# Kernel tuning notes

Hardware: AMD Instinct MI355X
Metric: run time of the kernel (lower is better)

Reference implementation:

```python
import jax, jax.numpy as jnp
import numpy as np

ATT_DIM = 128
C = 256
B, H, W = 4, 64, 64


def setup_inputs() -> dict:
    key = jax.random.key(0)
    ks = jax.random.split(key, 6)
    s = 1.0 / np.sqrt(C)
    return {
        "x": jax.random.normal(ks[0], (B, C, H, W), dtype=jnp.float32),
        "Wg": jax.random.normal(ks[1], (ATT_DIM, C), dtype=jnp.float32) * s,
        "Wf": jax.random.normal(ks[2], (ATT_DIM, C), dtype=jnp.float32) * s,
        "Wh": jax.random.normal(ks[3], (ATT_DIM, C), dtype=jnp.float32) * s,
        "Wv": jax.random.normal(ks[4], (C, ATT_DIM), dtype=jnp.float32) * (1.0 / np.sqrt(ATT_DIM)),
        "lambda_att": jax.random.normal(ks[5], (), dtype=jnp.float32),
    }


def reference(x, Wg, Wf, Wh, Wv, lambda_att):
    # x: [B, C, H, W]; 1x1 channels_first convs == channel matmuls
    b, c, h, w = x.shape
    hw = h * w
    d = Wg.shape[0]
    # project and flatten spatial dims -> tokens: [B, HW, d]
    g = jnp.einsum('dc,bchw->bhwd', Wg, x).reshape(b, hw, d)  # query
    f = jnp.einsum('dc,bchw->bhwd', Wf, x).reshape(b, hw, d)  # value
    hh = jnp.einsum('dc,bchw->bhwd', Wh, x).reshape(b, hw, d)  # key
    # keras layers.Attention([g, f, h]): scores = query @ key^T (unscaled),
    # out = softmax(scores) @ value
    scores = jnp.einsum('bqd,bkd->bqk', g, hh)  # [B, HW, HW]
    attw = jax.nn.softmax(scores, axis=-1)
    v = jnp.einsum('bqk,bkd->bqd', attw, f)  # [B, HW, d]
    # back to [B, d, H, W], project to C channels
    v = v.transpose(0, 2, 1).reshape(b, d, h, w)
    v = jnp.einsum('cd,bdhw->bchw', Wv, v)
    return x + lambda_att * v
```

## Files before the change

### kernel.cpp

```cpp
#include <hip/hip_runtime.h>

typedef _Float16 h16;
typedef __attribute__((ext_vector_type(8))) _Float16 half8;
typedef __attribute__((ext_vector_type(4))) _Float16 half4;
typedef __attribute__((ext_vector_type(4))) float f32x4;
typedef unsigned int u32;
typedef unsigned short u16;
typedef unsigned long long u64;

#define LOG2E 1.44269504088896340736f

__device__ __forceinline__ void gl_lds16(const void* g, void* l){
  __builtin_amdgcn_global_load_lds((const __attribute__((address_space(1))) u32*)g,
                                   (__attribute__((address_space(3))) u32*)l, 16, 0, 0);
}
__device__ __forceinline__ f32x4 mfma16(half8 a, half8 b, f32x4 c){
  return __builtin_amdgcn_mfma_f32_16x16x32_f16(a, b, c, 0, 0, 0);
}
__device__ __forceinline__ f32x4 fzero(){
  f32x4 z = {0.f, 0.f, 0.f, 0.f};
  return z;
}

__global__ void k_cvtw(const float* __restrict__ Wg, const float* __restrict__ Wf,
                       const float* __restrict__ Wh, const float* __restrict__ Wv,
                       h16* __restrict__ o){
  int i = blockIdx.x * 256 + threadIdx.x;
  o[i]          = (h16)Wg[i];
  o[32768 + i]  = (h16)Wf[i];
  o[65536 + i]  = (h16)Wh[i];
  o[98304 + i]  = (h16)Wv[i];
}

__global__ __launch_bounds__(256, 2)
void k_proj(const float* __restrict__ x, const h16* __restrict__ Wgb,
            const h16* __restrict__ Whb, const h16* __restrict__ Wfb,
            h16* __restrict__ Q, h16* __restrict__ K, h16* __restrict__ Vt){
  __shared__ __align__(16) char Xl[64 * 512];
  int bid = blockIdx.x;
  int b = bid >> 6, p0 = (bid & 63) * 64;
  int tid = threadIdx.x;
  int w = tid >> 6, lane = tid & 63, g4 = lane >> 4, ln = lane & 15;

  #pragma unroll
  for (int pass = 0; pass < 4; ++pass){
    int idx = pass * 256 + tid;
    int c4 = idx >> 4, p4 = idx & 15;
    const float* xp = x + ((size_t)b * 256 + c4 * 4) * 4096 + p0 + p4 * 4;
    float4 v0 = *(const float4*)(xp);
    float4 v1 = *(const float4*)(xp + 4096);
    float4 v2 = *(const float4*)(xp + 8192);
    float4 v3 = *(const float4*)(xp + 12288);
    #pragma unroll
    for (int i = 0; i < 4; ++i){
      int row = p4 * 4 + i;
      half4 v = { (h16)((&v0.x)[i]), (h16)((&v1.x)[i]),
                  (h16)((&v2.x)[i]), (h16)((&v3.x)[i]) };
      *(half4*)&Xl[row * 512 + ((c4 * 8) ^ ((row & 7) << 4))] = v;
    }
  }
  __syncthreads();

  half8 xf[4][8];
  #pragma unroll
  for (int pt = 0; pt < 4; ++pt){
    int p = pt * 16 + ln;
    #pragma unroll
    for (int ks = 0; ks < 8; ++ks)
      xf[pt][ks] = *(const half8*)&Xl[p * 512 + (((ks * 4 + g4) ^ (p & 7)) << 4)];
  }

  const h16* Ws0[3] = {Wgb, Whb, Wfb};
  #pragma unroll
  for (int mat = 0; mat < 3; ++mat){
    const h16* Wm = Ws0[mat];
    #pragma unroll
    for (int dtl = 0; dtl < 2; ++dtl){
      int drow = w * 32 + dtl * 16 + ln;
      half8 wf[8];
      #pragma unroll
      for (int ks = 0; ks < 8; ++ks)
        wf[ks] = *(const half8*)&Wm[(size_t)drow * 256 + ks * 32 + g4 * 8];
      #pragma unroll
      for (int pt = 0; pt < 4; ++pt){
        f32x4 acc = fzero();
        #pragma unroll
        for (int ks = 0; ks < 8; ++ks)
          acc = mfma16(wf[ks], xf[pt][ks], acc);
        int p = p0 + pt * 16 + ln;
        int dbase = w * 32 + dtl * 16 + g4 * 4;
        if (mat < 2){
          h16* Dst = (mat == 0) ? Q : K;
          half4 v = { (h16)acc[0], (h16)acc[1], (h16)acc[2], (h16)acc[3] };
          *(half4*)&Dst[((size_t)b * 4096 + p) * 128 + dbase] = v;
        } else {
          #pragma unroll
          for (int r = 0; r < 4; ++r)
            Vt[((size_t)b * 128 + dbase + r) * 4096 + p] = (h16)acc[r];
        }
      }
    }
  }
}

__global__ __launch_bounds__(128, 2)
void k_attn(const h16* __restrict__ Q, const h16* __restrict__ K,
            const h16* __restrict__ Vt, h16* __restrict__ Opart,
            float* __restrict__ Mb, float* __restrict__ Lb){
  __shared__ __align__(16) char Kl[16384];
  __shared__ __align__(16) char Vl[16384];
  __shared__ __align__(16) char Pl[2][4096];

  int bid = blockIdx.x;
  int b = bid >> 8, qb = (bid >> 2) & 63, sp = bid & 3;
  int tid = threadIdx.x;
  int w = tid >> 6, lane = tid & 63, g4 = lane >> 4, ln = lane & 15;
  int q0 = qb * 64 + w * 32;

  half8 qf[2][4];
  #pragma unroll
  for (int qt = 0; qt < 2; ++qt)
    #pragma unroll
    for (int ks = 0; ks < 4; ++ks)
      qf[qt][ks] = *(const half8*)&Q[((size_t)b * 4096 + q0 + qt * 16 + ln) * 128 + ks * 32 + g4 * 8];

  f32x4 acc[2][8];
  #pragma unroll
  for (int qt = 0; qt < 2; ++qt)
    #pragma unroll
    for (int dt = 0; dt < 8; ++dt)
      acc[qt][dt] = fzero();
  float mrow[2] = {-1e30f, -1e30f};
  float lrow[2] = {0.f, 0.f};

  for (int t = 0; t < 16; ++t){
    int kv0 = sp * 1024 + t * 64;
    __syncthreads();
    #pragma unroll
    for (int i = 0; i < 8; ++i){
      int off = i * 2048 + w * 1024 + lane * 16;
      int row = off >> 8, c16 = (off >> 4) & 15;
      gl_lds16(&K[((size_t)b * 4096 + kv0 + row) * 128 + ((c16 ^ (row & 7)) << 3)],
               &Kl[i * 2048 + w * 1024]);
    }
    #pragma unroll
    for (int i = 0; i < 8; ++i){
      int off = i * 2048 + w * 1024 + lane * 16;
      int row = off >> 7, c16 = (off >> 4) & 7;
      gl_lds16(&Vt[((size_t)b * 128 + row) * 4096 + kv0 + ((c16 ^ (row & 7)) << 3)],
               &Vl[i * 2048 + w * 1024]);
    }
    __syncthreads();

    f32x4 s[4][2];
    #pragma unroll
    for (int kt = 0; kt < 4; ++kt)
      #pragma unroll
      for (int qt = 0; qt < 2; ++qt) s[kt][qt] = fzero();
    #pragma unroll
    for (int kt = 0; kt < 4; ++kt){
      int key = kt * 16 + ln;
      #pragma unroll
      for (int ks = 0; ks < 4; ++ks){
        half8 kf = *(const half8*)&Kl[key * 256 + (((ks * 4 + g4) ^ (key & 7)) << 4)];
        #pragma unroll
        for (int qt = 0; qt < 2; ++qt)
          s[kt][qt] = mfma16(kf, qf[qt][ks], s[kt][qt]);
      }
    }

    #pragma unroll
    for (int qt = 0; qt < 2; ++qt){
      float mx = -1e30f;
      #pragma unroll
      for (int kt = 0; kt < 4; ++kt)
        #pragma unroll
        for (int r = 0; r < 4; ++r) mx = fmaxf(mx, s[kt][qt][r]);
      mx = fmaxf(mx, __shfl_xor(mx, 16));
      mx = fmaxf(mx, __shfl_xor(mx, 32));
      float mnew = fmaxf(mrow[qt], mx);
      float scale = exp2f((mrow[qt] - mnew) * LOG2E);
      mrow[qt] = mnew;
      float ps = 0.f;
      int q = qt * 16 + ln;
      #pragma unroll
      for (int kt = 0; kt < 4; ++kt){
        float e0 = exp2f((s[kt][qt][0] - mnew) * LOG2E);
        float e1 = exp2f((s[kt][qt][1] - mnew) * LOG2E);
        float e2 = exp2f((s[kt][qt][2] - mnew) * LOG2E);
        float e3 = exp2f((s[kt][qt][3] - mnew) * LOG2E);
        ps += (e0 + e1) + (e2 + e3);
        half4 pv = { (h16)e0, (h16)e1, (h16)e2, (h16)e3 };
        *(half4*)&Pl[w][q * 128 + ((kt * 32 + g4 * 8) ^ ((q & 7) << 4))] = pv;
      }
      ps += __shfl_xor(ps, 16);
      ps += __shfl_xor(ps, 32);
      lrow[qt] = lrow[qt] * scale + ps;
      #pragma unroll
      for (int r = 0; r < 4; ++r){
        float sc = __shfl(scale, g4 * 4 + r);
        #pragma unroll
        for (int dt = 0; dt < 8; ++dt) acc[qt][dt][r] *= sc;
      }
    }

    #pragma unroll
    for (int st = 0; st < 2; ++st){
      half8 pa[2];
      #pragma unroll
      for (int qt = 0; qt < 2; ++qt){
        int q = qt * 16 + ln;
        pa[qt] = *(const half8*)&Pl[w][q * 128 + (((st * 4 + g4) ^ (q & 7)) << 4)];
      }
      #pragma unroll
      for (int dt = 0; dt < 8; ++dt){
        int row = dt * 16 + ln;
        half8 vf = *(const half8*)&Vl[row * 128 + (((st * 4 + g4) ^ (row & 7)) << 4)];
        #pragma unroll
        for (int qt = 0; qt < 2; ++qt)
          acc[qt][dt] = mfma16(pa[qt], vf, acc[qt][dt]);
      }
    }
  }

  int pb = (b * 64 + qb) * 4 + sp;
  #pragma unroll
  for (int qt = 0; qt < 2; ++qt)
    #pragma unroll
    for (int dt = 0; dt < 8; ++dt)
      #pragma unroll
      for (int r = 0; r < 4; ++r){
        int qloc = w * 32 + qt * 16 + g4 * 4 + r;
        Opart[(size_t)pb * 8192 + qloc * 128 + dt * 16 + ln] = (h16)acc[qt][dt][r];
      }
  if (lane < 16){
    #pragma unroll
    for (int qt = 0; qt < 2; ++qt){
      int qloc = w * 32 + qt * 16 + lane;
      Mb[pb * 64 + qloc] = mrow[qt];
      Lb[pb * 64 + qloc] = lrow[qt];
    }
  }
}

__global__ __launch_bounds__(256, 4)
void k_comb(const h16* __restrict__ Opart, const float* __restrict__ Mb,
            const float* __restrict__ Lb, h16* __restrict__ O){
  int bid = blockIdx.x;
  int b = bid >> 6, qb = bid & 63;
  int tid = threadIdx.x;
  int q = tid >> 2, dg = tid & 3;
  int base = bid * 4;
  float m0 = Mb[(base + 0) * 64 + q], m1 = Mb[(base + 1) * 64 + q];
  float m2 = Mb[(base + 2) * 64 + q], m3 = Mb[(base + 3) * 64 + q];
  float mmax = fmaxf(fmaxf(m0, m1), fmaxf(m2, m3));
  float w0 = exp2f((m0 - mmax) * LOG2E), w1 = exp2f((m1 - mmax) * LOG2E);
  float w2 = exp2f((m2 - mmax) * LOG2E), w3 = exp2f((m3 - mmax) * LOG2E);
  float denom = w0 * Lb[(base + 0) * 64 + q] + w1 * Lb[(base + 1) * 64 + q]
              + w2 * Lb[(base + 2) * 64 + q] + w3 * Lb[(base + 3) * 64 + q];
  float inv = 1.f / denom;
  #pragma unroll
  for (int d8 = 0; d8 < 4; ++d8){
    int d = dg * 32 + d8 * 8;
    half8 a0 = *(const half8*)&Opart[((size_t)(base + 0) * 64 + q) * 128 + d];
    half8 a1 = *(const half8*)&Opart[((size_t)(base + 1) * 64 + q) * 128 + d];
    half8 a2 = *(const half8*)&Opart[((size_t)(base + 2) * 64 + q) * 128 + d];
    half8 a3 = *(const half8*)&Opart[((size_t)(base + 3) * 64 + q) * 128 + d];
    half8 o;
    #pragma unroll
    for (int j = 0; j < 8; ++j){
      float v = w0 * (float)a0[j] + w1 * (float)a1[j]
              + w2 * (float)a2[j] + w3 * (float)a3[j];
      o[j] = (h16)(v * inv);
    }
    *(half8*)&O[((size_t)b * 4096 + qb * 64 + q) * 128 + d] = o;
  }
}

__global__ __launch_bounds__(256, 2)
void k_oproj(const float* __restrict__ x, const h16* __restrict__ Wvb,
             const h16* __restrict__ O, const float* __restrict__ lamp,
             float* __restrict__ y){
  __shared__ __align__(16) char Ol[16384];
  int bid = blockIdx.x;
  int b = bid >> 6, p0 = (bid & 63) * 64;
  int tid = threadIdx.x;
  int w = tid >> 6, lane = tid & 63, g4 = lane >> 4, ln = lane & 15;
  float lam = lamp[0];

  #pragma unroll
  for (int i = 0; i < 4; ++i){
    int off = i * 4096 + w * 1024 + lane * 16;
    int row = off >> 8, c16 = (off >> 4) & 15;
    gl_lds16(&O[((size_t)b * 4096 + p0 + row) * 128 + ((c16 ^ (row & 7)) << 3)],
             &Ol[i * 4096 + w * 1024]);
  }
  __syncthreads();

  half8 of[4][4];
  #pragma unroll
  for (int pt = 0; pt < 4; ++pt){
    int p = pt * 16 + ln;
    #pragma unroll
    for (int ks = 0; ks < 4; ++ks)
      of[pt][ks] = *(const half8*)&Ol[p * 256 + (((ks * 4 + g4) ^ (p & 7)) << 4)];
  }
  #pragma unroll
  for (int ctl = 0; ctl < 4; ++ctl){
    int crow = w * 64 + ctl * 16 + ln;
    half8 wf[4];
    #pragma unroll
    for (int ks = 0; ks < 4; ++ks)
      wf[ks] = *(const half8*)&Wvb[(size_t)crow * 128 + ks * 32 + g4 * 8];
    #pragma unroll
    for (int pt = 0; pt < 4; ++pt){
      f32x4 a = fzero();
      #pragma unroll
      for (int ks = 0; ks < 4; ++ks) a = mfma16(wf[ks], of[pt][ks], a);
      int p = p0 + pt * 16 + ln;
      int c = w * 64 + ctl * 16 + g4 * 4;
      #pragma unroll
      for (int r = 0; r < 4; ++r){
        size_t idx = ((size_t)b * 256 + c + r) * 4096 + p;
        y[idx] = x[idx] + lam * a[r];
      }
    }
  }
}

extern "C" void kernel_launch(void* const* d_in, const int* in_sizes, int n_in,
                              void* d_out, int out_size, void* d_ws, size_t ws_size,
                              hipStream_t stream) {
  const float* x   = (const float*)d_in[0];
  const float* Wg  = (const float*)d_in[1];
  const float* Wf  = (const float*)d_in[2];
  const float* Wh  = (const float*)d_in[3];
  const float* Wv  = (const float*)d_in[4];
  const float* lam = (const float*)d_in[5];

  h16* Wall  = (h16*)d_ws;
  h16* Qb    = Wall + 131072;
  h16* Kb    = Qb + 2097152;
  h16* Vtb   = Kb + 2097152;
  h16* Ob    = Vtb + 2097152;
  h16* Opart = Ob + 2097152;
  float* Mb  = (float*)(Opart + 8388608);
  float* Lb  = Mb + 65536;

  k_cvtw<<<128, 256, 0, stream>>>(Wg, Wf, Wh, Wv, Wall);
  k_proj<<<256, 256, 0, stream>>>(x, Wall , Wall + 65536 , Wall + 32768 ,
                                  Qb, Kb, Vtb);
  k_attn<<<1024, 128, 0, stream>>>(Qb, Kb, Vtb, Opart, Mb, Lb);
  k_comb<<<256, 256, 0, stream>>>(Opart, Mb, Lb, Ob);
  k_oproj<<<256, 256, 0, stream>>>(x, Wall + 98304 , Ob, lam, (float*)d_out);
}
```

Baseline: 163.2 us.

## Double-buffer K tiles, read V from global, lazy rescale, fuse combine into oproj

The attention kernel now runs 4 waves of 16 query rows each. K tiles are double-buffered in LDS so the next tile's load overlaps compute, and V is read straight from global memory instead of being staged. Softmax rescaling is skipped unless the row max grows by more than 8, and partial outputs are normalized before being written. The split-combine kernel is folded into the output projection, which removes one launch and the O round trip. Reading V from global adds uncached global traffic, and the lazy-rescale threshold lets fp16 probabilities reach e^8, which is within fp16 range.

```diff
diff --git a/kernel.cpp b/kernel.cpp
--- a/kernel.cpp
+++ b/kernel.cpp
@@ -5,7 +5,6 @@
 typedef __attribute__((ext_vector_type(4))) _Float16 half4;
 typedef __attribute__((ext_vector_type(4))) float f32x4;
 typedef unsigned int u32;
-typedef unsigned short u16;
 typedef unsigned long long u64;
 
 #define LOG2E 1.44269504088896340736f
@@ -103,208 +102,169 @@
   }
 }
 
-__global__ __launch_bounds__(128, 2)
+__global__ __launch_bounds__(256, 4)
 void k_attn(const h16* __restrict__ Q, const h16* __restrict__ K,
             const h16* __restrict__ Vt, h16* __restrict__ Opart,
             float* __restrict__ Mb, float* __restrict__ Lb){
-  __shared__ __align__(16) char Kl[16384];
-  __shared__ __align__(16) char Vl[16384];
-  __shared__ __align__(16) char Pl[2][4096];
+  __shared__ __align__(16) char Kl[2][16384];
+  __shared__ __align__(16) char Pl[4][2048];
 
   int bid = blockIdx.x;
   int b = bid >> 8, qb = (bid >> 2) & 63, sp = bid & 3;
   int tid = threadIdx.x;
   int w = tid >> 6, lane = tid & 63, g4 = lane >> 4, ln = lane & 15;
-  int q0 = qb * 64 + w * 32;
-
-  half8 qf[2][4];
-  #pragma unroll
-  for (int qt = 0; qt < 2; ++qt)
-    #pragma unroll
-    for (int ks = 0; ks < 4; ++ks)
-      qf[qt][ks] = *(const half8*)&Q[((size_t)b * 4096 + q0 + qt * 16 + ln) * 128 + ks * 32 + g4 * 8];
-
-  f32x4 acc[2][8];
-  #pragma unroll
-  for (int qt = 0; qt < 2; ++qt)
-    #pragma unroll
-    for (int dt = 0; dt < 8; ++dt)
-      acc[qt][dt] = fzero();
-  float mrow[2] = {-1e30f, -1e30f};
-  float lrow[2] = {0.f, 0.f};
-
-  for (int t = 0; t < 16; ++t){
-    int kv0 = sp * 1024 + t * 64;
-    __syncthreads();
-    #pragma unroll
-    for (int i = 0; i < 8; ++i){
-      int off = i * 2048 + w * 1024 + lane * 16;
+  int q0 = qb * 64 + w * 16;
+
+  half8 qf[4];
+  #pragma unroll
+  for (int ks = 0; ks < 4; ++ks)
+    qf[ks] = *(const half8*)&Q[((size_t)b * 4096 + q0 + ln) * 128 + ks * 32 + g4 * 8];
+
+  f32x4 acc[8];
+  #pragma unroll
+  for (int dt = 0; dt < 8; ++dt) acc[dt] = fzero();
+  float mrow = -1e30f, lrow = 0.f;
+
+  int base0 = sp * 1024;
+  const h16* vb = Vt + (size_t)b * 128 * 4096;
+
+  auto stage = [&](int buf, int kv0){
+    #pragma unroll
+    for (int i = 0; i < 4; ++i){
+      int off = i * 4096 + w * 1024 + lane * 16;
       int row = off >> 8, c16 = (off >> 4) & 15;
       gl_lds16(&K[((size_t)b * 4096 + kv0 + row) * 128 + ((c16 ^ (row & 7)) << 3)],
-               &Kl[i * 2048 + w * 1024]);
-    }
-    #pragma unroll
-    for (int i = 0; i < 8; ++i){
-      int off = i * 2048 + w * 1024 + lane * 16;
-      int row = off >> 7, c16 = (off >> 4) & 7;
-      gl_lds16(&Vt[((size_t)b * 128 + row) * 4096 + kv0 + ((c16 ^ (row & 7)) << 3)],
-               &Vl[i * 2048 + w * 1024]);
-    }
-    __syncthreads();
-
-    f32x4 s[4][2];
-    #pragma unroll
-    for (int kt = 0; kt < 4; ++kt)
-      #pragma unroll
-      for (int qt = 0; qt < 2; ++qt) s[kt][qt] = fzero();
+               &Kl[buf][i * 4096 + w * 1024]);
+    }
+  };
+
+  stage(0, base0);
+  __syncthreads();
+
+  int cur = 0;
+  for (int t = 0; t < 16; ++t){
+    int kv0 = base0 + t * 64;
+    if (t < 15) stage(cur ^ 1, kv0 + 64);
+
+    f32x4 s[4];
+    #pragma unroll
+    for (int kt = 0; kt < 4; ++kt) s[kt] = fzero();
     #pragma unroll
     for (int kt = 0; kt < 4; ++kt){
       int key = kt * 16 + ln;
       #pragma unroll
       for (int ks = 0; ks < 4; ++ks){
-        half8 kf = *(const half8*)&Kl[key * 256 + (((ks * 4 + g4) ^ (key & 7)) << 4)];
-        #pragma unroll
-        for (int qt = 0; qt < 2; ++qt)
-          s[kt][qt] = mfma16(kf, qf[qt][ks], s[kt][qt]);
-      }
-    }
-
-    #pragma unroll
-    for (int qt = 0; qt < 2; ++qt){
-      float mx = -1e30f;
-      #pragma unroll
-      for (int kt = 0; kt < 4; ++kt)
-        #pragma unroll
-        for (int r = 0; r < 4; ++r) mx = fmaxf(mx, s[kt][qt][r]);
-      mx = fmaxf(mx, __shfl_xor(mx, 16));
-      mx = fmaxf(mx, __shfl_xor(mx, 32));
-      float mnew = fmaxf(mrow[qt], mx);
-      float scale = exp2f((mrow[qt] - mnew) * LOG2E);
-      mrow[qt] = mnew;
-      float ps = 0.f;
-      int q = qt * 16 + ln;
-      #pragma unroll
-      for (int kt = 0; kt < 4; ++kt){
-        float e0 = exp2f((s[kt][qt][0] - mnew) * LOG2E);
-        float e1 = exp2f((s[kt][qt][1] - mnew) * LOG2E);
-        float e2 = exp2f((s[kt][qt][2] - mnew) * LOG2E);
-        float e3 = exp2f((s[kt][qt][3] - mnew) * LOG2E);
-        ps += (e0 + e1) + (e2 + e3);
-        half4 pv = { (h16)e0, (h16)e1, (h16)e2, (h16)e3 };
-        *(half4*)&Pl[w][q * 128 + ((kt * 32 + g4 * 8) ^ ((q & 7) << 4))] = pv;
-      }
-      ps += __shfl_xor(ps, 16);
-      ps += __shfl_xor(ps, 32);
-      lrow[qt] = lrow[qt] * scale + ps;
+        half8 kf = *(const half8*)&Kl[cur][key * 256 + (((ks * 4 + g4) ^ (key & 7)) << 4)];
+        s[kt] = mfma16(kf, qf[ks], s[kt]);
+      }
+    }
+
+    float mx = -1e30f;
+    #pragma unroll
+    for (int kt = 0; kt < 4; ++kt)
+      #pragma unroll
+      for (int r = 0; r < 4; ++r) mx = fmaxf(mx, s[kt][r]);
+    mx = fmaxf(mx, __shfl_xor(mx, 16));
+    mx = fmaxf(mx, __shfl_xor(mx, 32));
+    if (!__all(mx <= mrow + 8.f)){
+      float mnew = fmaxf(mrow, mx);
+      float scale = exp2f((mrow - mnew) * LOG2E);
+      lrow *= scale;
       #pragma unroll
       for (int r = 0; r < 4; ++r){
         float sc = __shfl(scale, g4 * 4 + r);
         #pragma unroll
-        for (int dt = 0; dt < 8; ++dt) acc[qt][dt][r] *= sc;
-      }
-    }
+        for (int dt = 0; dt < 8; ++dt) acc[dt][r] *= sc;
+      }
+      mrow = mnew;
+    }
+    float ps = 0.f;
+    #pragma unroll
+    for (int kt = 0; kt < 4; ++kt){
+      float e0 = exp2f((s[kt][0] - mrow) * LOG2E);
+      float e1 = exp2f((s[kt][1] - mrow) * LOG2E);
+      float e2 = exp2f((s[kt][2] - mrow) * LOG2E);
+      float e3 = exp2f((s[kt][3] - mrow) * LOG2E);
+      ps += (e0 + e1) + (e2 + e3);
+      half4 pv = { (h16)e0, (h16)e1, (h16)e2, (h16)e3 };
+      *(half4*)&Pl[w][ln * 128 + ((kt * 32 + g4 * 8) ^ ((ln & 7) << 4))] = pv;
+    }
+    ps += __shfl_xor(ps, 16);
+    ps += __shfl_xor(ps, 32);
+    lrow += ps;
 
     #pragma unroll
     for (int st = 0; st < 2; ++st){
-      half8 pa[2];
-      #pragma unroll
-      for (int qt = 0; qt < 2; ++qt){
-        int q = qt * 16 + ln;
-        pa[qt] = *(const half8*)&Pl[w][q * 128 + (((st * 4 + g4) ^ (q & 7)) << 4)];
-      }
+      half8 pa = *(const half8*)&Pl[w][ln * 128 + (((st * 4 + g4) ^ (ln & 7)) << 4)];
       #pragma unroll
       for (int dt = 0; dt < 8; ++dt){
-        int row = dt * 16 + ln;
-        half8 vf = *(const half8*)&Vl[row * 128 + (((st * 4 + g4) ^ (row & 7)) << 4)];
-        #pragma unroll
-        for (int qt = 0; qt < 2; ++qt)
-          acc[qt][dt] = mfma16(pa[qt], vf, acc[qt][dt]);
-      }
-    }
-  }
-
+        half8 vf = *(const half8*)&vb[((size_t)(dt * 16 + ln)) * 4096 + kv0 + st * 32 + g4 * 8];
+        acc[dt] = mfma16(pa, vf, acc[dt]);
+      }
+    }
+
+    __syncthreads();
+    cur ^= 1;
+  }
+
+  float inv = 1.f / lrow;
   int pb = (b * 64 + qb) * 4 + sp;
   #pragma unroll
-  for (int qt = 0; qt < 2; ++qt)
+  for (int r = 0; r < 4; ++r){
+    float invr = __shfl(inv, g4 * 4 + r);
+    int qloc = w * 16 + g4 * 4 + r;
     #pragma unroll
     for (int dt = 0; dt < 8; ++dt)
-      #pragma unroll
-      for (int r = 0; r < 4; ++r){
-        int qloc = w * 32 + qt * 16 + g4 * 4 + r;
-        Opart[(size_t)pb * 8192 + qloc * 128 + dt * 16 + ln] = (h16)acc[qt][dt][r];
-      }
+      Opart[(size_t)pb * 8192 + qloc * 128 + dt * 16 + ln] = (h16)(acc[dt][r] * invr);
+  }
   if (lane < 16){
-    #pragma unroll
-    for (int qt = 0; qt < 2; ++qt){
-      int qloc = w * 32 + qt * 16 + lane;
-      Mb[pb * 64 + qloc] = mrow[qt];
-      Lb[pb * 64 + qloc] = lrow[qt];
-    }
-  }
-}
-
-__global__ __launch_bounds__(256, 4)
-void k_comb(const h16* __restrict__ Opart, const float* __restrict__ Mb,
-            const float* __restrict__ Lb, h16* __restrict__ O){
-  int bid = blockIdx.x;
-  int b = bid >> 6, qb = bid & 63;
-  int tid = threadIdx.x;
-  int q = tid >> 2, dg = tid & 3;
-  int base = bid * 4;
-  float m0 = Mb[(base + 0) * 64 + q], m1 = Mb[(base + 1) * 64 + q];
-  float m2 = Mb[(base + 2) * 64 + q], m3 = Mb[(base + 3) * 64 + q];
-  float mmax = fmaxf(fmaxf(m0, m1), fmaxf(m2, m3));
-  float w0 = exp2f((m0 - mmax) * LOG2E), w1 = exp2f((m1 - mmax) * LOG2E);
-  float w2 = exp2f((m2 - mmax) * LOG2E), w3 = exp2f((m3 - mmax) * LOG2E);
-  float denom = w0 * Lb[(base + 0) * 64 + q] + w1 * Lb[(base + 1) * 64 + q]
-              + w2 * Lb[(base + 2) * 64 + q] + w3 * Lb[(base + 3) * 64 + q];
-  float inv = 1.f / denom;
-  #pragma unroll
-  for (int d8 = 0; d8 < 4; ++d8){
-    int d = dg * 32 + d8 * 8;
-    half8 a0 = *(const half8*)&Opart[((size_t)(base + 0) * 64 + q) * 128 + d];
-    half8 a1 = *(const half8*)&Opart[((size_t)(base + 1) * 64 + q) * 128 + d];
-    half8 a2 = *(const half8*)&Opart[((size_t)(base + 2) * 64 + q) * 128 + d];
-    half8 a3 = *(const half8*)&Opart[((size_t)(base + 3) * 64 + q) * 128 + d];
-    half8 o;
-    #pragma unroll
-    for (int j = 0; j < 8; ++j){
-      float v = w0 * (float)a0[j] + w1 * (float)a1[j]
-              + w2 * (float)a2[j] + w3 * (float)a3[j];
-      o[j] = (h16)(v * inv);
-    }
-    *(half8*)&O[((size_t)b * 4096 + qb * 64 + q) * 128 + d] = o;
+    Mb[pb * 64 + w * 16 + lane] = mrow;
+    Lb[pb * 64 + w * 16 + lane] = lrow;
   }
 }
 
 __global__ __launch_bounds__(256, 2)
 void k_oproj(const float* __restrict__ x, const h16* __restrict__ Wvb,
-             const h16* __restrict__ O, const float* __restrict__ lamp,
+             const h16* __restrict__ Opart, const float* __restrict__ Mb,
+             const float* __restrict__ Lb, const float* __restrict__ lamp,
              float* __restrict__ y){
-  __shared__ __align__(16) char Ol[16384];
   int bid = blockIdx.x;
-  int b = bid >> 6, p0 = (bid & 63) * 64;
+  int b = bid >> 6, g64 = bid & 63;
+  int p0 = g64 * 64;
   int tid = threadIdx.x;
   int w = tid >> 6, lane = tid & 63, g4 = lane >> 4, ln = lane & 15;
   float lam = lamp[0];
-
-  #pragma unroll
-  for (int i = 0; i < 4; ++i){
-    int off = i * 4096 + w * 1024 + lane * 16;
-    int row = off >> 8, c16 = (off >> 4) & 15;
-    gl_lds16(&O[((size_t)b * 4096 + p0 + row) * 128 + ((c16 ^ (row & 7)) << 3)],
-             &Ol[i * 4096 + w * 1024]);
-  }
-  __syncthreads();
+  int base = (b * 64 + g64) * 4;
 
   half8 of[4][4];
   #pragma unroll
   for (int pt = 0; pt < 4; ++pt){
     int p = pt * 16 + ln;
-    #pragma unroll
-    for (int ks = 0; ks < 4; ++ks)
-      of[pt][ks] = *(const half8*)&Ol[p * 256 + (((ks * 4 + g4) ^ (p & 7)) << 4)];
-  }
+    float m0 = Mb[(base + 0) * 64 + p], m1 = Mb[(base + 1) * 64 + p];
+    float m2 = Mb[(base + 2) * 64 + p], m3 = Mb[(base + 3) * 64 + p];
+    float mmax = fmaxf(fmaxf(m0, m1), fmaxf(m2, m3));
+    float w0 = exp2f((m0 - mmax) * LOG2E) * Lb[(base + 0) * 64 + p];
+    float w1 = exp2f((m1 - mmax) * LOG2E) * Lb[(base + 1) * 64 + p];
+    float w2 = exp2f((m2 - mmax) * LOG2E) * Lb[(base + 2) * 64 + p];
+    float w3 = exp2f((m3 - mmax) * LOG2E) * Lb[(base + 3) * 64 + p];
+    float inv = 1.f / (w0 + w1 + w2 + w3);
+    w0 *= inv; w1 *= inv; w2 *= inv; w3 *= inv;
+    #pragma unroll
+    for (int ks = 0; ks < 4; ++ks){
+      size_t eo = (size_t)p * 128 + ks * 32 + g4 * 8;
+      half8 a0 = *(const half8*)&Opart[(size_t)(base + 0) * 8192 + eo];
+      half8 a1 = *(const half8*)&Opart[(size_t)(base + 1) * 8192 + eo];
+      half8 a2 = *(const half8*)&Opart[(size_t)(base + 2) * 8192 + eo];
+      half8 a3 = *(const half8*)&Opart[(size_t)(base + 3) * 8192 + eo];
+      half8 o;
+      #pragma unroll
+      for (int j = 0; j < 8; ++j)
+        o[j] = (h16)(w0 * (float)a0[j] + w1 * (float)a1[j]
+                   + w2 * (float)a2[j] + w3 * (float)a3[j]);
+      of[pt][ks] = o;
+    }
+  }
+
   #pragma unroll
   for (int ctl = 0; ctl < 4; ++ctl){
     int crow = w * 64 + ctl * 16 + ln;
@@ -342,15 +302,13 @@
   h16* Qb    = Wall + 131072;
   h16* Kb    = Qb + 2097152;
   h16* Vtb   = Kb + 2097152;
-  h16* Ob    = Vtb + 2097152;
-  h16* Opart = Ob + 2097152;
+  h16* Opart = Vtb + 2097152;
   float* Mb  = (float*)(Opart + 8388608);
   float* Lb  = Mb + 65536;
 
   k_cvtw<<<128, 256, 0, stream>>>(Wg, Wf, Wh, Wv, Wall);
   k_proj<<<256, 256, 0, stream>>>(x, Wall , Wall + 65536 , Wall + 32768 ,
                                   Qb, Kb, Vtb);
-  k_attn<<<1024, 128, 0, stream>>>(Qb, Kb, Vtb, Opart, Mb, Lb);
-  k_comb<<<256, 256, 0, stream>>>(Opart, Mb, Lb, Ob);
-  k_oproj<<<256, 256, 0, stream>>>(x, Wall + 98304 , Ob, lam, (float*)d_out);
-}
+  k_attn<<<1024, 256, 0, stream>>>(Qb, Kb, Vtb, Opart, Mb, Lb);
+  k_oproj<<<256, 256, 0, stream>>>(x, Wall + 98304 , Opart, Mb, Lb, lam, (float*)d_out);
+}
```

Result: slower. 227.2 us (+39.2%).
